# Kernel tuning notes

Measured on AMD Instinct MI355X. Metric: run time of the kernel, lower is better.

## Reference

```python
import jax, jax.numpy as jnp
import numpy as np

B, N, M = 16, 100000, 9  # batch, point_num, max_neighbor_num (slot 0 = self)


def setup_inputs() -> dict:
    key = jax.random.key(0)
    k1, k2, k3 = jax.random.split(key, 3)
    gt_pc = jax.random.normal(k1, (B, N, 3), dtype=jnp.float32)
    predict_pc = gt_pc + 0.1 * jax.random.normal(k2, (B, N, 3), dtype=jnp.float32)
    # neighbor ids in [0, N]; index N is the padding row (appended zero point)
    nb = jax.random.randint(k3, (N, M), 0, N + 1)
    nb = nb.at[:, 0].set(jnp.arange(N))  # slot 0 is the center vertex itself
    # degree = number of real (non-padding) neighbors
    neighbor_num = (nb[:, 1:] < N).sum(axis=1).astype(jnp.float32)
    return {
        "gt_pc": gt_pc,
        "predict_pc": predict_pc,
        "neighbor_id_lstlst": nb,
        "neighbor_num_lst": neighbor_num,
    }


def _laplacian(pc, neighbor_id_lstlst, neighbor_num_lst):
    # pc: [B, N, 3]; append a zero point so padding index N gathers zeros
    b = pc.shape[0]
    pc_ext = jnp.concatenate([pc, jnp.zeros((b, 1, 3), pc.dtype)], axis=1)  # [B, N+1, 3]
    g = pc_ext[:, neighbor_id_lstlst]  # [B, N, M, 3] gather of self + neighbors
    center = g[:, :, 0] * neighbor_num_lst[None, :, None]  # degree * x_i
    return center - g[:, :, 1:].sum(axis=2)  # deg*x_i - sum_j x_j


def reference(gt_pc, predict_pc, neighbor_id_lstlst, neighbor_num_lst):
    gt_lap = _laplacian(gt_pc, neighbor_id_lstlst, neighbor_num_lst)
    pr_lap = _laplacian(predict_pc, neighbor_id_lstlst, neighbor_num_lst)
    return jnp.abs(gt_lap - pr_lap).mean()
```

## Files before the change

kernel.cpp:

```cpp
#include <hip/hip_runtime.h>
#include <hip/hip_fp16.h>


#define NT 256
#define TI 128

union H4 {
  uint2 u;
  __half2 h[2];
};

__global__ __launch_bounds__(NT) void k1_diff_pack(
    const float* __restrict__ gt, const float* __restrict__ pr,
    uint2* __restrict__ d, float* __restrict__ out, int N) {
  __shared__ float sm[16][3 * TI + 1];
  const int t = threadIdx.x;
  const int i0 = blockIdx.x * TI;
  const int ni = min(TI, N - i0);
  const int nf = 3 * ni;

#pragma unroll
  for (int k = 0; k < (16 * 3 * TI) / (4 * NT); k++) {
    int f4 = t + k * NT;
    int b = f4 / (3 * TI / 4);
    int o4 = f4 - b * (3 * TI / 4);
    int off = o4 * 4;
    size_t gbase = ((size_t)b * N + i0) * 3;
    if (off + 4 <= nf) {
      float4 gv = *(const float4*)(gt + gbase + off);
      float4 pv = *(const float4*)(pr + gbase + off);
      sm[b][off + 0] = gv.x - pv.x;
      sm[b][off + 1] = gv.y - pv.y;
      sm[b][off + 2] = gv.z - pv.z;
      sm[b][off + 3] = gv.w - pv.w;
    } else {
#pragma unroll
      for (int c = 0; c < 4; c++) {
        int o = off + c;
        float v = 0.0f;
        if (o < nf) v = gt[gbase + o] - pr[gbase + o];
        sm[b][o] = v;
      }
    }
  }
  __syncthreads();

#pragma unroll
  for (int k = 0; k < (16 * TI) / NT; k++) {
    int el = t + k * NT;
    int il = el >> 4;
    int b = el & 15;
    if (il < ni) {
      float x = sm[b][il * 3 + 0];
      float y = sm[b][il * 3 + 1];
      float z = sm[b][il * 3 + 2];
      H4 o;
      o.h[0] = __floats2half2_rn(x, y);
      o.h[1] = __floats2half2_rn(z, 0.0f);
      d[(size_t)(i0 + il) * 16 + b] = o.u;
    }
  }

  if (blockIdx.x == 0) {
    if (t < 16) { uint2 z; z.x = 0u; z.y = 0u; d[(size_t)N * 16 + t] = z; }
    if (t == 16) *out = 0.0f;
  }
}

__device__ __forceinline__ void unpack(uint2 v, float& x, float& y, float& z) {
  H4 c; c.u = v;
  float2 xy = __half22float2(c.h[0]);
  x = xy.x; y = xy.y;
  z = __half2float(__low2half(c.h[1]));
}

__global__ __launch_bounds__(NT) void k2_lap_loss(
    const uint2* __restrict__ dp, const int* __restrict__ nb,
    const float* __restrict__ nn, float* __restrict__ out, int N,
    float scale) {
  const int f = blockIdx.x * NT + threadIdx.x;
  const int g = f >> 4;
  const int b = f & 15;
  const int i0 = g * 4;
  float s = 0.0f;

  if (i0 + 3 < N) {
    int idx[4][8];
#pragma unroll
    for (int q = 0; q < 4; q++) {
      const int* r = nb + (size_t)(i0 + q) * 9 + 1;
#pragma unroll
      for (int j = 0; j < 8; j++) idx[q][j] = r[j];
    }
    float w[4];
#pragma unroll
    for (int q = 0; q < 4; q++) w[q] = nn[i0 + q];
    uint2 c[4];
#pragma unroll
    for (int q = 0; q < 4; q++) c[q] = dp[(size_t)(i0 + q) * 16 + b];
    uint2 v[4][8];
#pragma unroll
    for (int q = 0; q < 4; q++) {
#pragma unroll
      for (int j = 0; j < 8; j++) v[q][j] = dp[(size_t)idx[q][j] * 16 + b];
    }

#pragma unroll
    for (int q = 0; q < 4; q++) {
      float ax, ay, az;
      unpack(c[q], ax, ay, az);
      ax *= w[q]; ay *= w[q]; az *= w[q];
#pragma unroll
      for (int j = 0; j < 8; j++) {
        float x, y, z; unpack(v[q][j], x, y, z);
        ax -= x; ay -= y; az -= z;
      }
      s += fabsf(ax) + fabsf(ay) + fabsf(az);
    }
  } else if (i0 < N) {
    for (int q = 0; q < 4; q++) {
      int i = i0 + q;
      if (i >= N) break;
      const int* r = nb + (size_t)i * 9 + 1;
      int ia[8];
#pragma unroll
      for (int j = 0; j < 8; j++) ia[j] = r[j];
      float w = nn[i];
      uint2 cc = dp[(size_t)i * 16 + b];
      uint2 vv[8];
#pragma unroll
      for (int j = 0; j < 8; j++) vv[j] = dp[(size_t)ia[j] * 16 + b];
      float ax, ay, az;
      unpack(cc, ax, ay, az);
      ax *= w; ay *= w; az *= w;
#pragma unroll
      for (int j = 0; j < 8; j++) {
        float x, y, z; unpack(vv[j], x, y, z);
        ax -= x; ay -= y; az -= z;
      }
      s += fabsf(ax) + fabsf(ay) + fabsf(az);
    }
  }

#pragma unroll
  for (int off = 32; off > 0; off >>= 1) s += __shfl_down(s, off);
  __shared__ float sm[NT / 64];
  int lane = threadIdx.x & 63, wv = threadIdx.x >> 6;
  if (lane == 0) sm[wv] = s;
  __syncthreads();
  if (threadIdx.x == 0) {
    float tt = 0.0f;
#pragma unroll
    for (int k = 0; k < NT / 64; k++) tt += sm[k];
    atomicAdd(out, tt * scale);
  }
}

__global__ void k0_zero(float* __restrict__ out) {
  if (threadIdx.x == 0) *out = 0.0f;
}

__global__ __launch_bounds__(NT) void k2_direct(
    const float* __restrict__ gt, const float* __restrict__ pr,
    const int* __restrict__ nb, const float* __restrict__ nn,
    float* __restrict__ out, int N, int K, float scale) {
  int u = blockIdx.x * NT + threadIdx.x;
  float s = 0.0f;
  if (u < 16 * N) {
    int b = u / N;
    int i = u - b * N;
    size_t cidx = ((size_t)b * N + i) * 3;
    float w = nn[i];
    float ax = (gt[cidx] - pr[cidx]) * w;
    float ay = (gt[cidx + 1] - pr[cidx + 1]) * w;
    float az = (gt[cidx + 2] - pr[cidx + 2]) * w;
    const int* row = nb + (size_t)i * (K + 1) + 1;
    for (int j = 0; j < K; j++) {
      int idx = row[j];
      if (idx < N) {
        size_t p = ((size_t)b * N + idx) * 3;
        ax -= (gt[p] - pr[p]);
        ay -= (gt[p + 1] - pr[p + 1]);
        az -= (gt[p + 2] - pr[p + 2]);
      }
    }
    s = fabsf(ax) + fabsf(ay) + fabsf(az);
  }
#pragma unroll
  for (int off = 32; off > 0; off >>= 1) s += __shfl_down(s, off);
  __shared__ float sm[NT / 64];
  int lane = threadIdx.x & 63, wv = threadIdx.x >> 6;
  if (lane == 0) sm[wv] = s;
  __syncthreads();
  if (threadIdx.x == 0) {
    float tt = 0.0f;
#pragma unroll
    for (int k = 0; k < NT / 64; k++) tt += sm[k];
    atomicAdd(out, tt * scale);
  }
}

extern "C" void kernel_launch(void* const* d_in, const int* in_sizes, int n_in,
                              void* d_out, int out_size, void* d_ws, size_t ws_size,
                              hipStream_t stream) {
  const float* gt = (const float*)d_in[0];
  const float* pr = (const float*)d_in[1];
  const int*   nb = (const int*)d_in[2];
  const float* nn = (const float*)d_in[3];
  int N = in_sizes[3];
  int M = in_sizes[2] / N;
  int K = M - 1;

  float scale = 1.0f / (16.0f * (float)N * 3.0f);
  size_t need = (size_t)(N + 1) * 16 * sizeof(uint2);

  if (K == 8 && ws_size >= need) {
    uint2* d = (uint2*)d_ws;

    int b1 = (N + TI - 1) / TI;
    k1_diff_pack<<<b1, NT, 0, stream>>>(gt, pr, d, (float*)d_out, N);

    int groups = (N + 3) / 4;
    int b2 = ((size_t)groups * 16 + NT - 1) / NT;
    k2_lap_loss<<<b2, NT, 0, stream>>>(d, nb, nn, (float*)d_out, N, scale);
  } else {
    k0_zero<<<1, 64, 0, stream>>>((float*)d_out);
    int b2 = (16 * N + NT - 1) / NT;
    k2_direct<<<b2, NT, 0, stream>>>(gt, pr, nb, nn, (float*)d_out, N, K, scale);
  }
}
```

Before: 110.8 us.

## Split packed diff buffer into four batch-quarter planes for gather locality

The packed half-precision difference buffer is reorganized from one [N+1][16] array into four [N+1][4] planes, each holding a quarter of the batch. Each k2 block now handles one quarter, so a neighbor gather touches 32 bytes instead of 128, and the working set per plane is smaller and more cache-resident. Neighbor-index and degree loads use nontemporal hints. The cost is that neighbor indices are reread four times, once per quarter, and gathers are narrower per wavefront.

New measurement: 113.0 us. Within noise of the previous version (+1.9%).

```diff
diff --git a/kernel.cpp b/kernel.cpp
--- a/kernel.cpp
+++ b/kernel.cpp
@@ -3,7 +3,10 @@
 
 
 #define NT 256
-#define TI 128
+#define TI 256
+#define Q  4
+
+typedef float f32x4 __attribute__((ext_vector_type(4)));
 
 union H4 {
   uint2 u;
@@ -12,58 +15,63 @@
 
 __global__ __launch_bounds__(NT) void k1_diff_pack(
     const float* __restrict__ gt, const float* __restrict__ pr,
-    uint2* __restrict__ d, float* __restrict__ out, int N) {
-  __shared__ float sm[16][3 * TI + 1];
-  const int t = threadIdx.x;
-  const int i0 = blockIdx.x * TI;
+    uint2* __restrict__ dq, float* __restrict__ out, int N) {
+  __shared__ float sm[4][3 * TI + 1];
+  const int t4 = blockIdx.x & 3;
+  const int chunk = blockIdx.x >> 2;
+  const int i0 = chunk * TI;
   const int ni = min(TI, N - i0);
   const int nf = 3 * ni;
-
-#pragma unroll
-  for (int k = 0; k < (16 * 3 * TI) / (4 * NT); k++) {
-    int f4 = t + k * NT;
-    int b = f4 / (3 * TI / 4);
-    int o4 = f4 - b * (3 * TI / 4);
+  const int tid = threadIdx.x;
+
+#pragma unroll
+  for (int k = 0; k < (4 * 3 * TI) / (4 * NT); k++) {
+    int f4 = tid + k * NT;
+    int bs = f4 / (3 * TI / 4);
+    int o4 = f4 - bs * (3 * TI / 4);
     int off = o4 * 4;
-    size_t gbase = ((size_t)b * N + i0) * 3;
+    size_t gbase = ((size_t)(t4 * 4 + bs) * N + i0) * 3;
     if (off + 4 <= nf) {
-      float4 gv = *(const float4*)(gt + gbase + off);
-      float4 pv = *(const float4*)(pr + gbase + off);
-      sm[b][off + 0] = gv.x - pv.x;
-      sm[b][off + 1] = gv.y - pv.y;
-      sm[b][off + 2] = gv.z - pv.z;
-      sm[b][off + 3] = gv.w - pv.w;
+      f32x4 gv = __builtin_nontemporal_load((const f32x4*)(gt + gbase + off));
+      f32x4 pv = __builtin_nontemporal_load((const f32x4*)(pr + gbase + off));
+      sm[bs][off + 0] = gv.x - pv.x;
+      sm[bs][off + 1] = gv.y - pv.y;
+      sm[bs][off + 2] = gv.z - pv.z;
+      sm[bs][off + 3] = gv.w - pv.w;
     } else {
 #pragma unroll
       for (int c = 0; c < 4; c++) {
         int o = off + c;
         float v = 0.0f;
         if (o < nf) v = gt[gbase + o] - pr[gbase + o];
-        sm[b][o] = v;
+        sm[bs][o] = v;
       }
     }
   }
   __syncthreads();
 
 #pragma unroll
-  for (int k = 0; k < (16 * TI) / NT; k++) {
-    int el = t + k * NT;
-    int il = el >> 4;
-    int b = el & 15;
+  for (int k = 0; k < (4 * TI) / NT; k++) {
+    int el = tid + k * NT;
+    int il = el >> 2;
+    int bs = el & 3;
     if (il < ni) {
-      float x = sm[b][il * 3 + 0];
-      float y = sm[b][il * 3 + 1];
-      float z = sm[b][il * 3 + 2];
+      float x = sm[bs][il * 3 + 0];
+      float y = sm[bs][il * 3 + 1];
+      float z = sm[bs][il * 3 + 2];
       H4 o;
       o.h[0] = __floats2half2_rn(x, y);
       o.h[1] = __floats2half2_rn(z, 0.0f);
-      d[(size_t)(i0 + il) * 16 + b] = o.u;
-    }
-  }
-
-  if (blockIdx.x == 0) {
-    if (t < 16) { uint2 z; z.x = 0u; z.y = 0u; d[(size_t)N * 16 + t] = z; }
-    if (t == 16) *out = 0.0f;
+      dq[((size_t)t4 * (N + 1) + (i0 + il)) * 4 + bs] = o.u;
+    }
+  }
+
+  if (chunk == 0) {
+    if (tid < 4) {
+      uint2 z; z.x = 0u; z.y = 0u;
+      dq[((size_t)t4 * (N + 1) + N) * 4 + tid] = z;
+    }
+    if (t4 == 0 && tid == 4) *out = 0.0f;
   }
 }
 
@@ -75,83 +83,69 @@
 }
 
 __global__ __launch_bounds__(NT) void k2_lap_loss(
-    const uint2* __restrict__ dp, const int* __restrict__ nb,
+    const uint2* __restrict__ dq, const int* __restrict__ nb,
     const float* __restrict__ nn, float* __restrict__ out, int N,
     float scale) {
-  const int f = blockIdx.x * NT + threadIdx.x;
-  const int g = f >> 4;
-  const int b = f & 15;
-  const int i0 = g * 4;
+  const int t4 = blockIdx.x & 3;
+  const int chunk = blockIdx.x >> 2;
+  const int g = threadIdx.x >> 2;
+  const int bs = threadIdx.x & 3;
+  const uint2* dqt = dq + (size_t)t4 * (N + 1) * 4 + bs;
+  const int ibase = chunk * (64 * Q) + g;
+
+  int ii[Q]; bool val[Q];
+#pragma unroll
+  for (int q = 0; q < Q; q++) {
+    int i = ibase + q * 64;
+    val[q] = (i < N);
+    ii[q] = val[q] ? i : 0;
+  }
+
+  int idx[Q][8];
+#pragma unroll
+  for (int q = 0; q < Q; q++) {
+    const int* r = nb + (size_t)ii[q] * 9 + 1;
+#pragma unroll
+    for (int j = 0; j < 8; j++) idx[q][j] = __builtin_nontemporal_load(r + j);
+  }
+  float w[Q]; uint2 c[Q];
+#pragma unroll
+  for (int q = 0; q < Q; q++) {
+    w[q] = __builtin_nontemporal_load(nn + ii[q]);
+    c[q] = dqt[(size_t)ii[q] * 4];
+  }
+  uint2 v[Q][8];
+#pragma unroll
+  for (int q = 0; q < Q; q++) {
+#pragma unroll
+    for (int j = 0; j < 8; j++) v[q][j] = dqt[(size_t)idx[q][j] * 4];
+  }
+
   float s = 0.0f;
-
-  if (i0 + 3 < N) {
-    int idx[4][8];
-#pragma unroll
-    for (int q = 0; q < 4; q++) {
-      const int* r = nb + (size_t)(i0 + q) * 9 + 1;
-#pragma unroll
-      for (int j = 0; j < 8; j++) idx[q][j] = r[j];
-    }
-    float w[4];
-#pragma unroll
-    for (int q = 0; q < 4; q++) w[q] = nn[i0 + q];
-    uint2 c[4];
-#pragma unroll
-    for (int q = 0; q < 4; q++) c[q] = dp[(size_t)(i0 + q) * 16 + b];
-    uint2 v[4][8];
-#pragma unroll
-    for (int q = 0; q < 4; q++) {
-#pragma unroll
-      for (int j = 0; j < 8; j++) v[q][j] = dp[(size_t)idx[q][j] * 16 + b];
-    }
-
-#pragma unroll
-    for (int q = 0; q < 4; q++) {
-      float ax, ay, az;
-      unpack(c[q], ax, ay, az);
-      ax *= w[q]; ay *= w[q]; az *= w[q];
-#pragma unroll
-      for (int j = 0; j < 8; j++) {
-        float x, y, z; unpack(v[q][j], x, y, z);
-        ax -= x; ay -= y; az -= z;
-      }
-      s += fabsf(ax) + fabsf(ay) + fabsf(az);
-    }
-  } else if (i0 < N) {
-    for (int q = 0; q < 4; q++) {
-      int i = i0 + q;
-      if (i >= N) break;
-      const int* r = nb + (size_t)i * 9 + 1;
-      int ia[8];
-#pragma unroll
-      for (int j = 0; j < 8; j++) ia[j] = r[j];
-      float w = nn[i];
-      uint2 cc = dp[(size_t)i * 16 + b];
-      uint2 vv[8];
-#pragma unroll
-      for (int j = 0; j < 8; j++) vv[j] = dp[(size_t)ia[j] * 16 + b];
-      float ax, ay, az;
-      unpack(cc, ax, ay, az);
-      ax *= w; ay *= w; az *= w;
-#pragma unroll
-      for (int j = 0; j < 8; j++) {
-        float x, y, z; unpack(vv[j], x, y, z);
-        ax -= x; ay -= y; az -= z;
-      }
-      s += fabsf(ax) + fabsf(ay) + fabsf(az);
-    }
+#pragma unroll
+  for (int q = 0; q < Q; q++) {
+    float ax, ay, az;
+    unpack(c[q], ax, ay, az);
+    ax *= w[q]; ay *= w[q]; az *= w[q];
+#pragma unroll
+    for (int j = 0; j < 8; j++) {
+      float x, y, z; unpack(v[q][j], x, y, z);
+      ax -= x; ay -= y; az -= z;
+    }
+    float term = fabsf(ax) + fabsf(ay) + fabsf(az);
+    s += val[q] ? term : 0.0f;
   }
 
 #pragma unroll
   for (int off = 32; off > 0; off >>= 1) s += __shfl_down(s, off);
-  __shared__ float sm[NT / 64];
+  __shared__ float smr[NT / 64];
   int lane = threadIdx.x & 63, wv = threadIdx.x >> 6;
-  if (lane == 0) sm[wv] = s;
+  if (lane == 0) smr[wv] = s;
   __syncthreads();
   if (threadIdx.x == 0) {
     float tt = 0.0f;
 #pragma unroll
-    for (int k = 0; k < NT / 64; k++) tt += sm[k];
+    for (int k = 0; k < NT / 64; k++) tt += smr[k];
     atomicAdd(out, tt * scale);
   }
 }
@@ -163,10 +157,10 @@
 __global__ __launch_bounds__(NT) void k2_direct(
     const float* __restrict__ gt, const float* __restrict__ pr,
     const int* __restrict__ nb, const float* __restrict__ nn,
-    float* __restrict__ out, int N, int K, float scale) {
+    float* __restrict__ out, int N, int K, int B, float scale) {
   int u = blockIdx.x * NT + threadIdx.x;
   float s = 0.0f;
-  if (u < 16 * N) {
+  if (u < B * N) {
     int b = u / N;
     int i = u - b * N;
     size_t cidx = ((size_t)b * N + i) * 3;
@@ -188,14 +182,14 @@
   }
 #pragma unroll
   for (int off = 32; off > 0; off >>= 1) s += __shfl_down(s, off);
-  __shared__ float sm[NT / 64];
+  __shared__ float smr[NT / 64];
   int lane = threadIdx.x & 63, wv = threadIdx.x >> 6;
-  if (lane == 0) sm[wv] = s;
+  if (lane == 0) smr[wv] = s;
   __syncthreads();
   if (threadIdx.x == 0) {
     float tt = 0.0f;
 #pragma unroll
-    for (int k = 0; k < NT / 64; k++) tt += sm[k];
+    for (int k = 0; k < NT / 64; k++) tt += smr[k];
     atomicAdd(out, tt * scale);
   }
 }
@@ -210,22 +204,24 @@
   int N = in_sizes[3];
   int M = in_sizes[2] / N;
   int K = M - 1;
-
-  float scale = 1.0f / (16.0f * (float)N * 3.0f);
-  size_t need = (size_t)(N + 1) * 16 * sizeof(uint2);
-
-  if (K == 8 && ws_size >= need) {
-    uint2* d = (uint2*)d_ws;
-
-    int b1 = (N + TI - 1) / TI;
-    k1_diff_pack<<<b1, NT, 0, stream>>>(gt, pr, d, (float*)d_out, N);
-
-    int groups = (N + 3) / 4;
-    int b2 = ((size_t)groups * 16 + NT - 1) / NT;
-    k2_lap_loss<<<b2, NT, 0, stream>>>(d, nb, nn, (float*)d_out, N, scale);
+  int B = in_sizes[0] / (3 * N);
+
+  float scale = 1.0f / ((float)B * (float)N * 3.0f);
+  size_t need = (size_t)(N + 1) * 4 * 4 * sizeof(uint2);
+
+  if (K == 8 && B == 16 && (N % 4) == 0 && ws_size >= need) {
+    uint2* dq = (uint2*)d_ws;
+
+    int nchunk1 = (N + TI - 1) / TI;
+    k1_diff_pack<<<4 * nchunk1, NT, 0, stream>>>(gt, pr, dq, (float*)d_out, N);
+
+    int nchunk2 = (N + 64 * Q - 1) / (64 * Q);
+    k2_lap_loss<<<4 * nchunk2, NT, 0, stream>>>(dq, nb, nn, (float*)d_out, N,
+                                                scale);
   } else {
     k0_zero<<<1, 64, 0, stream>>>((float*)d_out);
-    int b2 = (16 * N + NT - 1) / NT;
-    k2_direct<<<b2, NT, 0, stream>>>(gt, pr, nb, nn, (float*)d_out, N, K, scale);
-  }
-}
+    int b2 = (B * N + NT - 1) / NT;
+    k2_direct<<<b2, NT, 0, stream>>>(gt, pr, nb, nn, (float*)d_out, N, K, B,
+                                     scale);
+  }
+}
```
